# Kernel tuning notes

Hardware: AMD Instinct MI355X
Metric: run time of the kernel (lower is better)

## Reference

```python
import jax, jax.numpy as jnp
import numpy as np

VOXEL_SIZE = np.array([0.2, 0.2, 4.0], dtype=np.float32)
PC_MIN = np.array([0.0, -40.0, -3.0], dtype=np.float32)
BN_EPS = 1e-3
N_POINTS = 1_500_000
N_VOXELS = 200_000
C_IN = 7   # (4 - 3) + 6 stats channels (cluster offset + voxel-center offset)
C_OUT = 64


def setup_inputs() -> dict:
    key = jax.random.key(0)
    ks = jax.random.split(key, 8)
    features = jax.random.normal(ks[0], (N_POINTS, 4), dtype=jnp.float32)
    point2voxel = jax.random.randint(ks[1], (N_POINTS,), 0, N_VOXELS).astype(jnp.int32)
    voxel_coors = jnp.stack([
        jax.random.randint(ks[2], (N_VOXELS,), 0, 2),    # batch idx
        jnp.zeros((N_VOXELS,), jnp.int32),               # z (pillars -> 0)
        jax.random.randint(ks[3], (N_VOXELS,), 0, 400),  # y bin
        jax.random.randint(ks[4], (N_VOXELS,), 0, 352),  # x bin
    ], axis=1).astype(jnp.int32)
    W = jax.random.normal(ks[5], (C_IN, C_OUT), dtype=jnp.float32) * 0.1
    bn_gamma = jnp.ones((C_OUT,), jnp.float32)
    bn_beta = jnp.zeros((C_OUT,), jnp.float32)
    bn_mean = jax.random.normal(ks[6], (C_OUT,), dtype=jnp.float32) * 0.01
    bn_var = jax.random.uniform(ks[7], (C_OUT,), minval=0.5, maxval=1.5, dtype=jnp.float32)
    return dict(features=features, W=W, bn_gamma=bn_gamma, bn_beta=bn_beta,
                bn_mean=bn_mean, bn_var=bn_var, point2voxel=point2voxel,
                voxel_coors=voxel_coors)


def reference(features, W, bn_gamma, bn_beta, bn_mean, bn_var, point2voxel, voxel_coors):
    M = voxel_coors.shape[0]
    xyz = features[:, :3]

    # --- stats: cluster-center offset (per-voxel mean of xyz, mapped back) ---
    cnt = jax.ops.segment_sum(jnp.ones((xyz.shape[0],), xyz.dtype), point2voxel,
                              num_segments=M)
    vmean = jax.ops.segment_sum(xyz, point2voxel, num_segments=M)
    vmean = vmean / jnp.maximum(cnt, 1.0)[:, None]
    cluster_off = xyz - vmean[point2voxel]

    # --- stats: voxel-center offset ---
    vs = jnp.asarray(VOXEL_SIZE)
    mn = jnp.asarray(PC_MIN)
    # coors layout is (batch, z, y, x) -> take (x, y, z)
    centers = (voxel_coors[:, jnp.array([3, 2, 1])].astype(jnp.float32) + 0.5) * vs + mn
    center_off = xyz - centers[point2voxel]

    feats = jnp.concatenate([cluster_off, center_off, features[:, 3:]], axis=-1)  # [N,7]

    # --- PFN layer: Linear(bias=False) + BN1d (eval stats) + ReLU ---
    h = feats @ W
    h = (h - bn_mean) * jax.lax.rsqrt(bn_var + BN_EPS) * bn_gamma + bn_beta
    h = jax.nn.relu(h)

    # --- scatter max-reduce to voxels ---
    vfeats = jax.ops.segment_max(h, point2voxel, num_segments=M)
    vfeats = jnp.where(jnp.isfinite(vfeats), vfeats, 0.0)  # guard rare empty voxels
    return vfeats, voxel_coors
```

## Files before the change

### kernel.cpp

```cpp
#include <hip/hip_runtime.h>


#define BBITS 8
#define BVOX  (1 << BBITS)
#define PCAP  4096
#define NBLK  256

__global__ __launch_bounds__(256) void hist_k(const int* __restrict__ p2v,
                                              int* __restrict__ mat,
                                              int N, int NB, int chunk) {
    __shared__ int h[1024];
    int b = blockIdx.x, tid = threadIdx.x;
    for (int k = tid; k < NB; k += 256) h[k] = 0;
    __syncthreads();
    int s = b * chunk, e = min(N, s + chunk);
    for (int i = s + tid; i < e; i += 256)
        atomicAdd(&h[p2v[i] >> BBITS], 1);
    __syncthreads();
    for (int k = tid; k < NB; k += 256) mat[k * NBLK + b] = h[k];
}

__global__ void scanA_k(int* __restrict__ a, int* __restrict__ bsum, int S) {
    __shared__ int s[256];
    int tid = threadIdx.x;
    int base = blockIdx.x * 1024 + tid * 4;
    int c0 = (base + 0 < S) ? a[base + 0] : 0;
    int c1 = (base + 1 < S) ? a[base + 1] : 0;
    int c2 = (base + 2 < S) ? a[base + 2] : 0;
    int c3 = (base + 3 < S) ? a[base + 3] : 0;
    int tsum = c0 + c1 + c2 + c3;
    s[tid] = tsum;
    __syncthreads();
    for (int off = 1; off < 256; off <<= 1) {
        int v = (tid >= off) ? s[tid - off] : 0;
        __syncthreads();
        s[tid] += v;
        __syncthreads();
    }
    int excl = s[tid] - tsum;
    if (base + 0 < S) a[base + 0] = excl;
    if (base + 1 < S) a[base + 1] = excl + c0;
    if (base + 2 < S) a[base + 2] = excl + c0 + c1;
    if (base + 3 < S) a[base + 3] = excl + c0 + c1 + c2;
    if (tid == 255) bsum[blockIdx.x] = s[255];
}

__global__ void scanB_k(int* __restrict__ bsum, int nb) {
    __shared__ int s[256];
    int tid = threadIdx.x;
    int v = (tid < nb) ? bsum[tid] : 0;
    s[tid] = v;
    __syncthreads();
    for (int off = 1; off < 256; off <<= 1) {
        int t = (tid >= off) ? s[tid - off] : 0;
        __syncthreads();
        s[tid] += t;
        __syncthreads();
    }
    if (tid < nb) bsum[tid] = s[tid] - v;
}

__global__ void scanC_k(int* __restrict__ a, const int* __restrict__ bsum, int S) {
    int i = blockIdx.x * blockDim.x + threadIdx.x;
    if (i < S) a[i] += bsum[i >> 10];
}

__global__ __launch_bounds__(256) void scatter_kidx_k(const int* __restrict__ p2v,
                                                      const int* __restrict__ mat,
                                                      int* __restrict__ keyidx,
                                                      int N, int NB, int chunk) {
    __shared__ int cur[1024];
    int b = blockIdx.x, tid = threadIdx.x;
    for (int k = tid; k < NB; k += 256) cur[k] = mat[k * NBLK + b];
    __syncthreads();
    int s = b * chunk, e = min(N, s + chunk);
    for (int i = s + tid; i < e; i += 256) {
        int v = p2v[i];
        int k = v >> BBITS;
        int pos = atomicAdd(&cur[k], 1);
        keyidx[pos] = (i << BBITS) | (v & (BVOX - 1));
    }
}

__global__ __launch_bounds__(256) void gather_bucket_k(
    const float4* __restrict__ feats, const int* __restrict__ keyidx,
    const int* __restrict__ mat, const float* __restrict__ W,
    const float* __restrict__ gamma, const float* __restrict__ beta,
    const float* __restrict__ mean, const float* __restrict__ var,
    const int* __restrict__ coors,
    float* __restrict__ out_v, float* __restrict__ out_c,
    int M, int NB, int N) {
    __shared__ float4 spay[PCAP];
    __shared__ int lcnt[BVOX];
    __shared__ int loff[BVOX];
    __shared__ int lcur[BVOX];

    int bk = blockIdx.x, tid = threadIdx.x;
    int lane = tid & 63, w = tid >> 6;

    float w0 = W[0 * 64 + lane], w1 = W[1 * 64 + lane], w2 = W[2 * 64 + lane];
    float w3 = W[3 * 64 + lane], w4 = W[4 * 64 + lane], w5 = W[5 * 64 + lane];
    float w6 = W[6 * 64 + lane];
    float u0 = w0 + w3, u1 = w1 + w4, u2 = w2 + w5, u3 = w6;
    float sc = gamma[lane] * rsqrtf(var[lane] + 1e-3f);
    float bi = beta[lane] - mean[lane] * sc;
    bool take_max = (sc >= 0.0f);

    int s = mat[bk * NBLK];
    int e = (bk + 1 < NB) ? mat[(bk + 1) * NBLK] : N;
    int L = e - s;
    if (L > PCAP) L = PCAP;

    int pk[16];
#pragma unroll
    for (int r = 0; r < 16; ++r) {
        int j = tid + r * 256;
        pk[r] = (j < L) ? keyidx[s + j] : -1;
    }

    lcnt[tid] = 0;
    __syncthreads();
#pragma unroll
    for (int r = 0; r < 16; ++r)
        if (pk[r] >= 0) atomicAdd(&lcnt[pk[r] & (BVOX - 1)], 1);
    __syncthreads();

    {
        int v = lcnt[tid];
        loff[tid] = v;
        __syncthreads();
        for (int off = 1; off < 256; off <<= 1) {
            int t = (tid >= off) ? loff[tid - off] : 0;
            __syncthreads();
            loff[tid] += t;
            __syncthreads();
        }
        int ex = loff[tid] - v;
        __syncthreads();
        loff[tid] = ex;
        lcur[tid] = ex;
    }
    __syncthreads();

    float4 fv[16];
#pragma unroll
    for (int r = 0; r < 16; ++r)
        if (pk[r] >= 0) fv[r] = feats[pk[r] >> BBITS];
#pragma unroll
    for (int r = 0; r < 16; ++r)
        if (pk[r] >= 0) {
            int pos = atomicAdd(&lcur[pk[r] & (BVOX - 1)], 1);
            spay[pos] = fv[r];
        }

    int vbase = bk << BBITS;
    int vend = min(M, vbase + BVOX);
    for (int j = tid; j < (vend - vbase) * 4; j += 256)
        out_c[(size_t)vbase * 4 + j] = (float)coors[(size_t)vbase * 4 + j];
    __syncthreads();

    for (int q = 0; q < 64; ++q) {
        int lv = (w << 6) + q;
        int v = vbase + lv;
        if (v >= M) break;
        int npts = lcnt[lv];
        int st = loff[lv];
        int c1 = coors[v * 4 + 1], c2 = coors[v * 4 + 2], c3 = coors[v * 4 + 3];
        float cx = (c3 + 0.5f) * 0.2f;
        float cy = (c2 + 0.5f) * 0.2f - 40.0f;
        float cz = (c1 + 0.5f) * 4.0f - 3.0f;
        float sx = 0.f, sy = 0.f, sz = 0.f;
        float amax = -3.402823466e+38f, amin = 3.402823466e+38f;
        int i = 0;
        for (; i + 3 < npts; i += 4) {
            float4 f0 = spay[st + i + 0];
            float4 f1 = spay[st + i + 1];
            float4 f2 = spay[st + i + 2];
            float4 f3 = spay[st + i + 3];
            sx += f0.x + f1.x + f2.x + f3.x;
            sy += f0.y + f1.y + f2.y + f3.y;
            sz += f0.z + f1.z + f2.z + f3.z;
            float a0 = f0.x * u0 + f0.y * u1 + f0.z * u2 + f0.w * u3;
            float a1 = f1.x * u0 + f1.y * u1 + f1.z * u2 + f1.w * u3;
            float a2 = f2.x * u0 + f2.y * u1 + f2.z * u2 + f2.w * u3;
            float a3 = f3.x * u0 + f3.y * u1 + f3.z * u2 + f3.w * u3;
            amax = fmaxf(fmaxf(fmaxf(amax, a0), fmaxf(a1, a2)), a3);
            amin = fminf(fminf(fminf(amin, a0), fminf(a1, a2)), a3);
        }
        for (; i < npts; ++i) {
            float4 f = spay[st + i];
            sx += f.x; sy += f.y; sz += f.z;
            float a = f.x * u0 + f.y * u1 + f.z * u2 + f.w * u3;
            amax = fmaxf(amax, a);
            amin = fminf(amin, a);
        }
        float res = 0.0f;
        if (npts > 0) {
            float inv = 1.0f / (float)npts;
            float mx = sx * inv, my = sy * inv, mz = sz * inv;
            float K = mx * w0 + my * w1 + mz * w2 + cx * w3 + cy * w4 + cz * w5;
            float aext = take_max ? amax : amin;
            res = fmaxf((aext - K) * sc + bi, 0.0f);
        }
        out_v[(size_t)v * 64 + lane] = res;
    }
}

extern "C" void kernel_launch(void* const* d_in, const int* in_sizes, int n_in,
                              void* d_out, int out_size, void* d_ws, size_t ws_size,
                              hipStream_t stream) {
    const float* features = (const float*)d_in[0];
    const float* W        = (const float*)d_in[1];
    const float* gamma    = (const float*)d_in[2];
    const float* beta     = (const float*)d_in[3];
    const float* mean     = (const float*)d_in[4];
    const float* var      = (const float*)d_in[5];
    const int*   p2v      = (const int*)d_in[6];
    const int*   coors    = (const int*)d_in[7];
    int N = in_sizes[0] / 4;
    int M = in_sizes[7] / 4;

    int NB = (M + BVOX - 1) >> BBITS;
    int S = NB * NBLK;
    int chunk = (N + NBLK - 1) / NBLK;

    int* mat    = (int*)d_ws;
    int* bsum   = mat + S;
    int* keyidx = bsum + 256;

    float* out_v = (float*)d_out;
    float* out_c = out_v + (size_t)M * 64;

    hist_k<<<NBLK, 256, 0, stream>>>(p2v, mat, N, NB, chunk);
    int nbA = (S + 1023) / 1024;
    scanA_k<<<nbA, 256, 0, stream>>>(mat, bsum, S);
    scanB_k<<<1, 256, 0, stream>>>(bsum, nbA);
    scanC_k<<<(S + 255) / 256, 256, 0, stream>>>(mat, bsum, S);
    scatter_kidx_k<<<NBLK, 256, 0, stream>>>(p2v, mat, keyidx, N, NB, chunk);
    gather_bucket_k<<<NB, 256, 0, stream>>>(
        (const float4*)features, keyidx, mat, W, gamma, beta, mean, var,
        coors, out_v, out_c, M, NB, N);
}
```

Baseline: 149.9 us.

## Restructure bucket kernel: sort indices not payloads, stream points per wave with prefetch

The gather now loads features before the local histogram, writes payloads to shared memory unsorted, and sorts only small packed index words into per-voxel order. Each wave then walks its 64 voxels' points as one flat stream, with a two-stage software prefetch of index and payload, and flushes each voxel's result when the voxel id changes. Voxel centers are computed once per voxel into shared memory, and coordinates are copied with a vectorized int4 load. PCAP drops from 4096 to 3072 to fit the extra index array in shared memory, which can drop points if a bucket exceeds that capacity, and the indirect payload reads may cause bank conflicts.

```diff
diff --git a/kernel.cpp b/kernel.cpp
--- a/kernel.cpp
+++ b/kernel.cpp
@@ -3,7 +3,8 @@
 
 #define BBITS 8
 #define BVOX  (1 << BBITS)
-#define PCAP  4096
+#define PCAP  3072
+#define NR    (PCAP / 256)
 #define NBLK  256
 
 __global__ __launch_bounds__(256) void hist_k(const int* __restrict__ p2v,
@@ -90,10 +91,12 @@
     const int* __restrict__ coors,
     float* __restrict__ out_v, float* __restrict__ out_c,
     int M, int NB, int N) {
-    __shared__ float4 spay[PCAP];
-    __shared__ int lcnt[BVOX];
-    __shared__ int loff[BVOX];
-    __shared__ int lcur[BVOX];
+    __shared__ float4 s_pay[PCAP];
+    __shared__ int    s_id[PCAP];
+    __shared__ int    s_cnt[BVOX];
+    __shared__ int    s_off[BVOX + 1];
+    __shared__ int    s_cur[BVOX];
+    __shared__ float4 s_cen[BVOX];
 
     int bk = blockIdx.x, tid = threadIdx.x;
     int lane = tid & 63, w = tid >> 6;
@@ -108,101 +111,140 @@
 
     int s = mat[bk * NBLK];
     int e = (bk + 1 < NB) ? mat[(bk + 1) * NBLK] : N;
-    int L = e - s;
-    if (L > PCAP) L = PCAP;
-
-    int pk[16];
-#pragma unroll
-    for (int r = 0; r < 16; ++r) {
+    int L = min(e - s, PCAP);
+
+    int pk[NR];
+#pragma unroll
+    for (int r = 0; r < NR; ++r) {
         int j = tid + r * 256;
         pk[r] = (j < L) ? keyidx[s + j] : -1;
     }
-
-    lcnt[tid] = 0;
-    __syncthreads();
-#pragma unroll
-    for (int r = 0; r < 16; ++r)
-        if (pk[r] >= 0) atomicAdd(&lcnt[pk[r] & (BVOX - 1)], 1);
+    float4 fv[NR];
+#pragma unroll
+    for (int r = 0; r < NR; ++r)
+        if (pk[r] >= 0) fv[r] = feats[pk[r] >> BBITS];
+
+    s_cnt[tid] = 0;
+    __syncthreads();
+#pragma unroll
+    for (int r = 0; r < NR; ++r)
+        if (pk[r] >= 0) atomicAdd(&s_cnt[pk[r] & (BVOX - 1)], 1);
     __syncthreads();
 
     {
-        int v = lcnt[tid];
-        loff[tid] = v;
+        int val = s_cnt[tid];
+        s_cur[tid] = val;
         __syncthreads();
         for (int off = 1; off < 256; off <<= 1) {
-            int t = (tid >= off) ? loff[tid - off] : 0;
+            int t = (tid >= off) ? s_cur[tid - off] : 0;
             __syncthreads();
-            loff[tid] += t;
+            s_cur[tid] += t;
             __syncthreads();
         }
-        int ex = loff[tid] - v;
-        __syncthreads();
-        loff[tid] = ex;
-        lcur[tid] = ex;
-    }
-    __syncthreads();
-
-    float4 fv[16];
-#pragma unroll
-    for (int r = 0; r < 16; ++r)
-        if (pk[r] >= 0) fv[r] = feats[pk[r] >> BBITS];
-#pragma unroll
-    for (int r = 0; r < 16; ++r)
+        int ex = s_cur[tid] - val;
+        __syncthreads();
+        s_off[tid] = ex;
+        s_cur[tid] = ex;
+        if (tid == 255) s_off[BVOX] = ex + val;
+    }
+
+    int vbase = bk << BBITS;
+    int vg = vbase + tid;
+    if (vg < M) {
+        int4 cc = ((const int4*)coors)[vg];
+        ((float4*)out_c)[vg] = make_float4((float)cc.x, (float)cc.y,
+                                           (float)cc.z, (float)cc.w);
+        s_cen[tid] = make_float4((cc.w + 0.5f) * 0.2f,
+                                 (cc.z + 0.5f) * 0.2f - 40.0f,
+                                 (cc.y + 0.5f) * 4.0f - 3.0f, 0.0f);
+    }
+    __syncthreads();
+
+#pragma unroll
+    for (int r = 0; r < NR; ++r) {
+        int j = tid + r * 256;
+        if (pk[r] >= 0) s_pay[j] = fv[r];
+    }
+#pragma unroll
+    for (int r = 0; r < NR; ++r)
         if (pk[r] >= 0) {
-            int pos = atomicAdd(&lcur[pk[r] & (BVOX - 1)], 1);
-            spay[pos] = fv[r];
-        }
-
-    int vbase = bk << BBITS;
-    int vend = min(M, vbase + BVOX);
-    for (int j = tid; j < (vend - vbase) * 4; j += 256)
-        out_c[(size_t)vbase * 4 + j] = (float)coors[(size_t)vbase * 4 + j];
-    __syncthreads();
-
-    for (int q = 0; q < 64; ++q) {
-        int lv = (w << 6) + q;
-        int v = vbase + lv;
-        if (v >= M) break;
-        int npts = lcnt[lv];
-        int st = loff[lv];
-        int c1 = coors[v * 4 + 1], c2 = coors[v * 4 + 2], c3 = coors[v * 4 + 3];
-        float cx = (c3 + 0.5f) * 0.2f;
-        float cy = (c2 + 0.5f) * 0.2f - 40.0f;
-        float cz = (c1 + 0.5f) * 4.0f - 3.0f;
-        float sx = 0.f, sy = 0.f, sz = 0.f;
-        float amax = -3.402823466e+38f, amin = 3.402823466e+38f;
-        int i = 0;
-        for (; i + 3 < npts; i += 4) {
-            float4 f0 = spay[st + i + 0];
-            float4 f1 = spay[st + i + 1];
-            float4 f2 = spay[st + i + 2];
-            float4 f3 = spay[st + i + 3];
-            sx += f0.x + f1.x + f2.x + f3.x;
-            sy += f0.y + f1.y + f2.y + f3.y;
-            sz += f0.z + f1.z + f2.z + f3.z;
-            float a0 = f0.x * u0 + f0.y * u1 + f0.z * u2 + f0.w * u3;
-            float a1 = f1.x * u0 + f1.y * u1 + f1.z * u2 + f1.w * u3;
-            float a2 = f2.x * u0 + f2.y * u1 + f2.z * u2 + f2.w * u3;
-            float a3 = f3.x * u0 + f3.y * u1 + f3.z * u2 + f3.w * u3;
-            amax = fmaxf(fmaxf(fmaxf(amax, a0), fmaxf(a1, a2)), a3);
-            amin = fminf(fminf(fminf(amin, a0), fminf(a1, a2)), a3);
-        }
-        for (; i < npts; ++i) {
-            float4 f = spay[st + i];
-            sx += f.x; sy += f.y; sz += f.z;
-            float a = f.x * u0 + f.y * u1 + f.z * u2 + f.w * u3;
-            amax = fmaxf(amax, a);
-            amin = fminf(amin, a);
-        }
-        float res = 0.0f;
-        if (npts > 0) {
-            float inv = 1.0f / (float)npts;
-            float mx = sx * inv, my = sy * inv, mz = sz * inv;
-            float K = mx * w0 + my * w1 + mz * w2 + cx * w3 + cy * w4 + cz * w5;
-            float aext = take_max ? amax : amin;
-            res = fmaxf((aext - K) * sc + bi, 0.0f);
-        }
-        out_v[(size_t)v * 64 + lane] = res;
+            int vox = pk[r] & (BVOX - 1);
+            int pos = atomicAdd(&s_cur[vox], 1);
+            s_id[pos] = ((tid + r * 256) << BBITS) | vox;
+        }
+    __syncthreads();
+
+    int lv0 = w << 6;
+    int pstart = s_off[lv0], pend = s_off[lv0 + 64];
+
+    int cur = lv0 - 1;
+    float cnt_r = 0.f, sx = 0.f, sy = 0.f, sz = 0.f;
+    float amax = -3.402823466e+38f, amin = 3.402823466e+38f;
+    float4 cen = make_float4(0.f, 0.f, 0.f, 0.f);
+
+    auto flush = [&]() {
+        float inv = 1.0f / cnt_r;
+        float mx = sx * inv, my = sy * inv, mz = sz * inv;
+        float K = mx * w0 + my * w1 + mz * w2 +
+                  cen.x * w3 + cen.y * w4 + cen.z * w5;
+        float aext = take_max ? amax : amin;
+        out_v[(size_t)(vbase + cur) * 64 + lane] =
+            fmaxf((aext - K) * sc + bi, 0.0f);
+    };
+    auto proc = [&](int svj, float4 f) {
+        int vox = svj & (BVOX - 1);
+        if (vox != cur) {
+            if (cur >= lv0) flush();
+            for (int g = cur + 1; g < vox; ++g) {
+                int v = vbase + g;
+                if (v < M) out_v[(size_t)v * 64 + lane] = 0.0f;
+            }
+            cur = vox;
+            cen = s_cen[vox];
+            cnt_r = 0.f; sx = 0.f; sy = 0.f; sz = 0.f;
+            amax = -3.402823466e+38f; amin = 3.402823466e+38f;
+        }
+        cnt_r += 1.0f;
+        sx += f.x; sy += f.y; sz += f.z;
+        float a = f.x * u0 + f.y * u1 + f.z * u2 + f.w * u3;
+        amax = fmaxf(amax, a);
+        amin = fminf(amin, a);
+    };
+
+#define LD_S(base, sv)                                   \
+    _Pragma("unroll") for (int j = 0; j < 4; ++j) {      \
+        int t = (base) + j;                              \
+        sv[j] = (t < pend) ? s_id[t] : -1;               \
+    }
+
+    int svP[4], svL[4], svN[4];
+    float4 pfP[4] = {}, pfL[4] = {};
+    int i = pstart;
+    LD_S(i, svP);
+#pragma unroll
+    for (int j = 0; j < 4; ++j)
+        if (svP[j] >= 0) pfP[j] = s_pay[svP[j] >> BBITS];
+    LD_S(i + 4, svL);
+    while (i < pend) {
+#pragma unroll
+        for (int j = 0; j < 4; ++j)
+            if (svL[j] >= 0) pfL[j] = s_pay[svL[j] >> BBITS];
+        LD_S(i + 8, svN);
+#pragma unroll
+        for (int j = 0; j < 4; ++j)
+            if (svP[j] >= 0) proc(svP[j], pfP[j]);
+#pragma unroll
+        for (int j = 0; j < 4; ++j) {
+            svP[j] = svL[j]; svL[j] = svN[j]; pfP[j] = pfL[j];
+        }
+        i += 4;
+    }
+#undef LD_S
+
+    if (cur >= lv0) flush();
+    for (int g = cur + 1; g < lv0 + 64; ++g) {
+        int v = vbase + g;
+        if (v < M) out_v[(size_t)v * 64 + lane] = 0.0f;
     }
 }
 
```

New measurement: 228.7 us. 1.53x slower.

## Shrink voxel buckets to 64 per block and use wave-level prefix scan

Applied to the files above, without the earlier changes.

Reduces the bucket size from 256 to 64 voxels, so the gather kernel launches many more small blocks with a 768-point shared payload and a launch-bounds occupancy hint. The radix histogram/scatter now uses 64 partition blocks with up to 3200 buckets. The local offset scan becomes a single-wave shuffle scan, and voxel centers are precomputed once into shared memory alongside a vectorized coors-to-float copy. Buckets with more than 768 points would be silently truncated, which relies on the expected density of the inputs.

```diff
diff --git a/kernel.cpp b/kernel.cpp
--- a/kernel.cpp
+++ b/kernel.cpp
@@ -1,15 +1,17 @@
 #include <hip/hip_runtime.h>
 
 
-#define BBITS 8
+#define BBITS 6
 #define BVOX  (1 << BBITS)
-#define PCAP  4096
-#define NBLK  256
+#define PCAP  768
+#define NR    (PCAP / 256)
+#define NBLK  64
+#define BMAX  3200
 
 __global__ __launch_bounds__(256) void hist_k(const int* __restrict__ p2v,
                                               int* __restrict__ mat,
                                               int N, int NB, int chunk) {
-    __shared__ int h[1024];
+    __shared__ int h[BMAX];
     int b = blockIdx.x, tid = threadIdx.x;
     for (int k = tid; k < NB; k += 256) h[k] = 0;
     __syncthreads();
@@ -69,7 +71,7 @@
                                                       const int* __restrict__ mat,
                                                       int* __restrict__ keyidx,
                                                       int N, int NB, int chunk) {
-    __shared__ int cur[1024];
+    __shared__ int cur[BMAX];
     int b = blockIdx.x, tid = threadIdx.x;
     for (int k = tid; k < NB; k += 256) cur[k] = mat[k * NBLK + b];
     __syncthreads();
@@ -82,7 +84,7 @@
     }
 }
 
-__global__ __launch_bounds__(256) void gather_bucket_k(
+__global__ __launch_bounds__(256, 4) void gather_bucket_k(
     const float4* __restrict__ feats, const int* __restrict__ keyidx,
     const int* __restrict__ mat, const float* __restrict__ W,
     const float* __restrict__ gamma, const float* __restrict__ beta,
@@ -90,10 +92,11 @@
     const int* __restrict__ coors,
     float* __restrict__ out_v, float* __restrict__ out_c,
     int M, int NB, int N) {
-    __shared__ float4 spay[PCAP];
-    __shared__ int lcnt[BVOX];
-    __shared__ int loff[BVOX];
-    __shared__ int lcur[BVOX];
+    __shared__ float4 s_pay[PCAP];
+    __shared__ int    s_cnt[BVOX];
+    __shared__ int    s_off[BVOX];
+    __shared__ int    s_cur[BVOX];
+    __shared__ float4 s_cen[BVOX];
 
     int bk = blockIdx.x, tid = threadIdx.x;
     int lane = tid & 63, w = tid >> 6;
@@ -108,75 +111,80 @@
 
     int s = mat[bk * NBLK];
     int e = (bk + 1 < NB) ? mat[(bk + 1) * NBLK] : N;
-    int L = e - s;
-    if (L > PCAP) L = PCAP;
-
-    int pk[16];
-#pragma unroll
-    for (int r = 0; r < 16; ++r) {
+    int L = min(e - s, PCAP);
+
+    int pk[NR];
+    float4 fv[NR];
+#pragma unroll
+    for (int r = 0; r < NR; ++r) {
         int j = tid + r * 256;
         pk[r] = (j < L) ? keyidx[s + j] : -1;
     }
-
-    lcnt[tid] = 0;
-    __syncthreads();
-#pragma unroll
-    for (int r = 0; r < 16; ++r)
-        if (pk[r] >= 0) atomicAdd(&lcnt[pk[r] & (BVOX - 1)], 1);
-    __syncthreads();
-
-    {
-        int v = lcnt[tid];
-        loff[tid] = v;
-        __syncthreads();
-        for (int off = 1; off < 256; off <<= 1) {
-            int t = (tid >= off) ? loff[tid - off] : 0;
-            __syncthreads();
-            loff[tid] += t;
-            __syncthreads();
-        }
-        int ex = loff[tid] - v;
-        __syncthreads();
-        loff[tid] = ex;
-        lcur[tid] = ex;
-    }
-    __syncthreads();
-
-    float4 fv[16];
-#pragma unroll
-    for (int r = 0; r < 16; ++r)
+#pragma unroll
+    for (int r = 0; r < NR; ++r)
         if (pk[r] >= 0) fv[r] = feats[pk[r] >> BBITS];
-#pragma unroll
-    for (int r = 0; r < 16; ++r)
+
+    if (tid < BVOX) s_cnt[tid] = 0;
+    __syncthreads();
+#pragma unroll
+    for (int r = 0; r < NR; ++r)
+        if (pk[r] >= 0) atomicAdd(&s_cnt[pk[r] & (BVOX - 1)], 1);
+
+    int vbase = bk << BBITS;
+    if (tid < BVOX) {
+        int vg = vbase + tid;
+        if (vg < M) {
+            int4 cc = ((const int4*)coors)[vg];
+            ((float4*)out_c)[vg] = make_float4((float)cc.x, (float)cc.y,
+                                               (float)cc.z, (float)cc.w);
+            s_cen[tid] = make_float4((cc.w + 0.5f) * 0.2f,
+                                     (cc.z + 0.5f) * 0.2f - 40.0f,
+                                     (cc.y + 0.5f) * 4.0f - 3.0f, 0.0f);
+        }
+    }
+    __syncthreads();
+
+    if (w == 0) {
+        int c = s_cnt[lane];
+        int x = c;
+        for (int off = 1; off < 64; off <<= 1) {
+            int t = __shfl_up(x, off);
+            if (lane >= off) x += t;
+        }
+        int ex = x - c;
+        s_off[lane] = ex;
+        s_cur[lane] = ex;
+    }
+    __syncthreads();
+
+#pragma unroll
+    for (int r = 0; r < NR; ++r)
         if (pk[r] >= 0) {
-            int pos = atomicAdd(&lcur[pk[r] & (BVOX - 1)], 1);
-            spay[pos] = fv[r];
-        }
-
-    int vbase = bk << BBITS;
-    int vend = min(M, vbase + BVOX);
-    for (int j = tid; j < (vend - vbase) * 4; j += 256)
-        out_c[(size_t)vbase * 4 + j] = (float)coors[(size_t)vbase * 4 + j];
-    __syncthreads();
-
-    for (int q = 0; q < 64; ++q) {
-        int lv = (w << 6) + q;
+            int vox = pk[r] & (BVOX - 1);
+            int pos = atomicAdd(&s_cur[vox], 1);
+            s_pay[pos] = fv[r];
+        }
+    __syncthreads();
+
+    int lv0 = w << 4;
+    int cnts[16];
+#pragma unroll
+    for (int q = 0; q < 16; ++q) cnts[q] = s_cnt[lv0 + q];
+    int st = s_off[lv0];
+
+    for (int q = 0; q < 16; ++q) {
+        int lv = lv0 + q;
         int v = vbase + lv;
-        if (v >= M) break;
-        int npts = lcnt[lv];
-        int st = loff[lv];
-        int c1 = coors[v * 4 + 1], c2 = coors[v * 4 + 2], c3 = coors[v * 4 + 3];
-        float cx = (c3 + 0.5f) * 0.2f;
-        float cy = (c2 + 0.5f) * 0.2f - 40.0f;
-        float cz = (c1 + 0.5f) * 4.0f - 3.0f;
+        int npts = cnts[q];
+        float4 cen = s_cen[lv];
         float sx = 0.f, sy = 0.f, sz = 0.f;
         float amax = -3.402823466e+38f, amin = 3.402823466e+38f;
         int i = 0;
         for (; i + 3 < npts; i += 4) {
-            float4 f0 = spay[st + i + 0];
-            float4 f1 = spay[st + i + 1];
-            float4 f2 = spay[st + i + 2];
-            float4 f3 = spay[st + i + 3];
+            float4 f0 = s_pay[st + i + 0];
+            float4 f1 = s_pay[st + i + 1];
+            float4 f2 = s_pay[st + i + 2];
+            float4 f3 = s_pay[st + i + 3];
             sx += f0.x + f1.x + f2.x + f3.x;
             sy += f0.y + f1.y + f2.y + f3.y;
             sz += f0.z + f1.z + f2.z + f3.z;
@@ -188,7 +196,7 @@
             amin = fminf(fminf(fminf(amin, a0), fminf(a1, a2)), a3);
         }
         for (; i < npts; ++i) {
-            float4 f = spay[st + i];
+            float4 f = s_pay[st + i];
             sx += f.x; sy += f.y; sz += f.z;
             float a = f.x * u0 + f.y * u1 + f.z * u2 + f.w * u3;
             amax = fmaxf(amax, a);
@@ -198,11 +206,13 @@
         if (npts > 0) {
             float inv = 1.0f / (float)npts;
             float mx = sx * inv, my = sy * inv, mz = sz * inv;
-            float K = mx * w0 + my * w1 + mz * w2 + cx * w3 + cy * w4 + cz * w5;
+            float K = mx * w0 + my * w1 + mz * w2 +
+                      cen.x * w3 + cen.y * w4 + cen.z * w5;
             float aext = take_max ? amax : amin;
             res = fmaxf((aext - K) * sc + bi, 0.0f);
         }
-        out_v[(size_t)v * 64 + lane] = res;
+        if (v < M) out_v[(size_t)v * 64 + lane] = res;
+        st += npts;
     }
 }
 
```

New measurement: 145.2 us. 3.1% less time.
